# Kernel tuning notes

Measured on AMD Instinct MI355X. Metric: run time of the kernel, lower is better.

## Reference

```python
import jax, jax.numpy as jnp
import numpy as np

B, T, E, D, H = 32, 2048, 1024, 1024, 1024


def setup_inputs() -> dict:
    key = jax.random.key(0)
    ks = jax.random.split(key, 8)
    s_e = 1.0 / np.sqrt(E)
    s_d = 1.0 / np.sqrt(D)
    s_h = 1.0 / np.sqrt(H)
    return {
        "enc": jax.random.normal(ks[0], (B, T, E), dtype=jnp.float32),
        "dec": jax.random.normal(ks[1], (B, D), dtype=jnp.float32),
        "inp_mask": jnp.ones((B, T), dtype=jnp.float32),
        "W_enc": jax.random.uniform(ks[2], (E, H), jnp.float32, -s_e, s_e),
        "b_enc": jax.random.uniform(ks[3], (H,), jnp.float32, -s_e, s_e),
        "W_dec": jax.random.uniform(ks[4], (D, H), jnp.float32, -s_d, s_d),
        "b_dec": jax.random.uniform(ks[5], (H,), jnp.float32, -s_d, s_d),
        "w_out": jax.random.uniform(ks[6], (H,), jnp.float32, -s_h, s_h),
        "b_out": jax.random.uniform(ks[7], (), jnp.float32, -s_h, s_h),
    }


def reference(enc, dec, inp_mask, W_enc, b_enc, W_dec, b_dec, w_out, b_out):
    # hidden_enc: [B, T, H]; hidden_dec broadcast as query: [B, 1, H]
    hidden_enc = jnp.einsum("bte,eh->bth", enc, W_enc) + b_enc
    hidden_dec = dec @ W_dec + b_dec
    # additive attention score: tanh(h_enc + h_dec) . w_out + b_out -> [B, T]
    logits = jnp.tanh(hidden_enc + hidden_dec[:, None, :]) @ w_out + b_out
    logits = jnp.where(inp_mask > 0, logits, jnp.float32(-1e9))
    probs = jax.nn.softmax(logits, axis=-1)  # [B, T]
    attn = jnp.einsum("bt,bte->be", probs, enc)  # weighted sum of enc
    return attn, probs
```

## Files before the change

### kernel.cpp

```cpp
#include <hip/hip_runtime.h>

#define B_ 32
#define T_ 2048
#define E_ 1024
#define H_ 1024
#define M_ (B_*T_)

typedef __attribute__((ext_vector_type(8))) short short8;
typedef __attribute__((ext_vector_type(4))) float f32x4;


__device__ __forceinline__ void gload_lds16(const void* g, void* l) {
  __builtin_amdgcn_global_load_lds(
      (const __attribute__((address_space(1))) void*)g,
      (__attribute__((address_space(3))) void*)l, 16, 0, 0);
}

__device__ __forceinline__ short f2bf(float x) {
  unsigned u = __float_as_uint(x);
  unsigned r = (u + 0x7fffu + ((u >> 16) & 1u)) >> 16;
  return (short)r;
}

__device__ __forceinline__ float fast_tanh(float x) {
  float e = __expf(2.f * x);
  return 1.f - 2.f / (e + 1.f);
}


__global__ __launch_bounds__(256) void k0_wt(const float* __restrict__ W,
                                             unsigned short* __restrict__ Wt) {
  __shared__ float t[32][33];
  int e0 = (blockIdx.x >> 5) << 5;
  int h0 = (blockIdx.x & 31) << 5;
  int r = threadIdx.x >> 5, c = threadIdx.x & 31;
#pragma unroll
  for (int i = 0; i < 4; ++i)
    t[r + i*8][c] = W[(size_t)(e0 + r + i*8) * H_ + h0 + c];
  __syncthreads();
#pragma unroll
  for (int i = 0; i < 4; ++i)
    Wt[(size_t)(h0 + r + i*8) * E_ + e0 + c] = (unsigned short)f2bf(t[c][r + i*8]);
}


__global__ __launch_bounds__(256) void k1_cvec(const float* __restrict__ dec,
                                               const float* __restrict__ Wd,
                                               const float* __restrict__ b_enc,
                                               const float* __restrict__ b_dec,
                                               float* __restrict__ cvec) {
  __shared__ float ds[1024];
  int b = blockIdx.x >> 2, hb = blockIdx.x & 3;
  int tid = threadIdx.x;
#pragma unroll
  for (int i = 0; i < 4; ++i) ds[tid + i*256] = dec[b*1024 + tid + i*256];
  __syncthreads();
  int h = hb*256 + tid;
  float acc = b_enc[h] + b_dec[h];
#pragma unroll 8
  for (int d = 0; d < 1024; ++d) acc += ds[d] * Wd[(size_t)d * H_ + h];
  cvec[b*H_ + h] = acc;
}


__global__ __launch_bounds__(256) void k2_logits(
    const float* __restrict__ enc,
    const unsigned short* __restrict__ Wt,
    const float* __restrict__ cvec,
    const float* __restrict__ w_out,
    float* __restrict__ logits)
{
  __shared__ float ldsA[128*32];
  __shared__ unsigned short ldsB[128*32];

  const int tid  = threadIdx.x;
  const int wave = tid >> 6, lane = tid & 63;
  const int lr = lane & 15, lk = lane >> 4;
  const int wr = wave >> 1, wc = wave & 1;
  const int bm = blockIdx.x >> 3, bn = blockIdx.x & 7;

  const float* asrc[4];
  void* adst[4];
#pragma unroll
  for (int i = 0; i < 4; ++i) {
    int pos  = i*4096 + wave*1024 + lane*16;
    int row  = pos >> 7;
    int slot = (pos >> 4) & 7;
    int ks   = (slot ^ (row & 7)) * 4;
    asrc[i] = enc + (size_t)(bm*128 + row) * E_ + ks;
    adst[i] = (char*)ldsA + i*4096 + wave*1024;
  }
  const unsigned short* bsrc[2];
  void* bdst[2];
#pragma unroll
  for (int i = 0; i < 2; ++i) {
    int pos  = i*4096 + wave*1024 + lane*16;
    int nrow = pos >> 6;
    int ke   = (pos & 63) >> 1;
    bsrc[i] = Wt + (size_t)(bn*128 + nrow) * E_ + ke;
    bdst[i] = (char*)ldsB + i*4096 + wave*1024;
  }

  f32x4 acc[4][4];
  {
    f32x4 z = {0.f, 0.f, 0.f, 0.f};
#pragma unroll
    for (int mi = 0; mi < 4; ++mi)
#pragma unroll
      for (int ni = 0; ni < 4; ++ni) acc[mi][ni] = z;
  }

  for (int kt = 0; kt < E_/32; ++kt) {
    if (kt) __syncthreads();
#pragma unroll
    for (int i = 0; i < 4; ++i) gload_lds16(asrc[i] + kt*32, adst[i]);
#pragma unroll
    for (int i = 0; i < 2; ++i) gload_lds16(bsrc[i] + kt*32, bdst[i]);
    __syncthreads();

    short8 bfr[4];
#pragma unroll
    for (int ni = 0; ni < 4; ++ni) {
      int nrow = wc*64 + ni*16 + lr;
      bfr[ni] = *(const short8*)((const char*)ldsB + nrow*64 + lk*16);
    }
    short8 afr[4];
#pragma unroll
    for (int mi = 0; mi < 4; ++mi) {
      int row = wr*64 + mi*16 + lr;
      int s1 = (2*lk)     ^ (row & 7);
      int s2 = (2*lk + 1) ^ (row & 7);
      f32x4 f1 = *(const f32x4*)((const char*)ldsA + row*128 + s1*16);
      f32x4 f2 = *(const f32x4*)((const char*)ldsA + row*128 + s2*16);
      short8 a;
      a[0] = f2bf(f1[0]); a[1] = f2bf(f1[1]); a[2] = f2bf(f1[2]); a[3] = f2bf(f1[3]);
      a[4] = f2bf(f2[0]); a[5] = f2bf(f2[1]); a[6] = f2bf(f2[2]); a[7] = f2bf(f2[3]);
      afr[mi] = a;
    }
#pragma unroll
    for (int mi = 0; mi < 4; ++mi)
#pragma unroll
      for (int ni = 0; ni < 4; ++ni)
        acc[mi][ni] = __builtin_amdgcn_mfma_f32_16x16x32_bf16(
            afr[mi], bfr[ni], acc[mi][ni], 0, 0, 0);
  }

  const int bIdx = bm >> 4;
  float cv[4], wv[4];
#pragma unroll
  for (int ni = 0; ni < 4; ++ni) {
    int n = bn*128 + wc*64 + ni*16 + lr;
    cv[ni] = cvec[bIdx*H_ + n];
    wv[ni] = w_out[n];
  }
#pragma unroll
  for (int mi = 0; mi < 4; ++mi) {
#pragma unroll
    for (int r = 0; r < 4; ++r) {
      float s = 0.f;
#pragma unroll
      for (int ni = 0; ni < 4; ++ni) {
        float h = acc[mi][ni][r] + cv[ni];
        s += wv[ni] * fast_tanh(h);
      }
      s += __shfl_xor(s, 1);
      s += __shfl_xor(s, 2);
      s += __shfl_xor(s, 4);
      s += __shfl_xor(s, 8);
      if (lr == 0) {
        int m = bm*128 + wr*64 + mi*16 + lk*4 + r;
        atomicAdd(&logits[m], s);
      }
    }
  }
}


__global__ __launch_bounds__(256) void k3_softmax(
    const float* __restrict__ logits, const float* __restrict__ mask,
    const float* __restrict__ b_out, float* __restrict__ probs) {
  __shared__ float redm[4], reds[4];
  int b = blockIdx.x, tid = threadIdx.x;
  int wave = tid >> 6, lane = tid & 63;
  float bo = b_out[0];
  float lg[8];
  float mx = -1e30f;
#pragma unroll
  for (int i = 0; i < 8; ++i) {
    int t = i*256 + tid;
    float v = logits[b*T_ + t] + bo;
    v = (mask[b*T_ + t] > 0.f) ? v : -1e9f;
    lg[i] = v;
    mx = fmaxf(mx, v);
  }
#pragma unroll
  for (int off = 32; off; off >>= 1) mx = fmaxf(mx, __shfl_xor(mx, off));
  if (lane == 0) redm[wave] = mx;
  __syncthreads();
  mx = fmaxf(fmaxf(redm[0], redm[1]), fmaxf(redm[2], redm[3]));
  float sum = 0.f;
#pragma unroll
  for (int i = 0; i < 8; ++i) { lg[i] = __expf(lg[i] - mx); sum += lg[i]; }
#pragma unroll
  for (int off = 32; off; off >>= 1) sum += __shfl_xor(sum, off);
  if (lane == 0) reds[wave] = sum;
  __syncthreads();
  sum = reds[0] + reds[1] + reds[2] + reds[3];
  float inv = 1.f / sum;
#pragma unroll
  for (int i = 0; i < 8; ++i) {
    int t = i*256 + tid;
    probs[b*T_ + t] = lg[i] * inv;
  }
}


__global__ __launch_bounds__(256) void k4_attn(const float* __restrict__ enc,
                                               const float* __restrict__ probs,
                                               float* __restrict__ attn) {
  int bb = blockIdx.x >> 6;
  int t0 = (blockIdx.x & 63) * 32;
  int e0 = threadIdx.x * 4;
  float a0 = 0.f, a1 = 0.f, a2 = 0.f, a3 = 0.f;
#pragma unroll 4
  for (int tt = 0; tt < 32; ++tt) {
    int t = t0 + tt;
    float p = probs[bb*T_ + t];
    f32x4 v = *(const f32x4*)(enc + ((size_t)bb*T_ + t)*E_ + e0);
    a0 += p*v[0]; a1 += p*v[1]; a2 += p*v[2]; a3 += p*v[3];
  }
  atomicAdd(&attn[bb*E_ + e0 + 0], a0);
  atomicAdd(&attn[bb*E_ + e0 + 1], a1);
  atomicAdd(&attn[bb*E_ + e0 + 2], a2);
  atomicAdd(&attn[bb*E_ + e0 + 3], a3);
}


extern "C" void kernel_launch(void* const* d_in, const int* in_sizes, int n_in,
                              void* d_out, int out_size, void* d_ws, size_t ws_size,
                              hipStream_t stream) {
  const float* enc   = (const float*)d_in[0];
  const float* dec   = (const float*)d_in[1];
  const float* mask  = (const float*)d_in[2];
  const float* W_enc = (const float*)d_in[3];
  const float* b_enc = (const float*)d_in[4];
  const float* W_dec = (const float*)d_in[5];
  const float* b_dec = (const float*)d_in[6];
  const float* w_out = (const float*)d_in[7];
  const float* b_out = (const float*)d_in[8];

  float* out   = (float*)d_out;
  float* attn  = out;
  float* probs = out + B_*E_;

  char* ws = (char*)d_ws;
  unsigned short* Wt = (unsigned short*)ws;
  float* cvec   = (float*)(ws + (2u<<20));
  float* logits = (float*)(ws + (2u<<20) + (128u<<10));

  hipMemsetAsync(logits, 0, M_*sizeof(float), stream);
  hipMemsetAsync(attn,   0, B_*E_*sizeof(float), stream);

  k0_wt     <<<1024, 256, 0, stream>>>(W_enc, Wt);
  k1_cvec   <<< 128, 256, 0, stream>>>(dec, W_dec, b_enc, b_dec, cvec);
  k2_logits <<<4096, 256, 0, stream>>>(enc, Wt, cvec, w_out, logits);
  k3_softmax<<<  B_, 256, 0, stream>>>(logits, mask, b_out, probs);
  k4_attn   <<<2048, 256, 0, stream>>>(enc, probs, attn);
}
```

Measured before the change: 728.8 us.

## Pre-convert enc to bf16, widen K tile to 64, swizzle blocks, coarsen attn

Adds a pass that converts enc to bf16 in workspace when there is room. The logits GEMM then streams bf16 A tiles straight into LDS with a K step of 64, so per-tile fp32 loads and repeated in-loop conversion go away. Without room, a fallback converts in registers before storing to LDS. The change also remaps block order so consecutive blocks reuse the same Wt tile, and gives each attention block four times more rows so fewer atomics are needed. The extra conversion pass adds a full read of enc plus a bf16 write, which may cost more than it saves.

```diff
diff --git a/kernel.cpp b/kernel.cpp
--- a/kernel.cpp
+++ b/kernel.cpp
@@ -41,6 +41,21 @@
 #pragma unroll
   for (int i = 0; i < 4; ++i)
     Wt[(size_t)(h0 + r + i*8) * E_ + e0 + c] = (unsigned short)f2bf(t[c][r + i*8]);
+}
+
+
+__global__ __launch_bounds__(256) void k0b_cvt(const float* __restrict__ src,
+                                               unsigned short* __restrict__ dst) {
+  size_t base = ((size_t)blockIdx.x * 256 + threadIdx.x) * 16;
+  const f32x4* s = (const f32x4*)(src + base);
+  f32x4 a = s[0], b = s[1], c = s[2], d = s[3];
+  short8 r0, r1;
+  r0[0]=f2bf(a[0]); r0[1]=f2bf(a[1]); r0[2]=f2bf(a[2]); r0[3]=f2bf(a[3]);
+  r0[4]=f2bf(b[0]); r0[5]=f2bf(b[1]); r0[6]=f2bf(b[2]); r0[7]=f2bf(b[3]);
+  r1[0]=f2bf(c[0]); r1[1]=f2bf(c[1]); r1[2]=f2bf(c[2]); r1[3]=f2bf(c[3]);
+  r1[4]=f2bf(d[0]); r1[5]=f2bf(d[1]); r1[6]=f2bf(d[2]); r1[7]=f2bf(d[3]);
+  *(short8*)(dst + base)     = r0;
+  *(short8*)(dst + base + 8) = r1;
 }
 
 
@@ -63,41 +78,41 @@
 }
 
 
+template<bool PRECVT>
 __global__ __launch_bounds__(256) void k2_logits(
     const float* __restrict__ enc,
+    const unsigned short* __restrict__ encbf,
     const unsigned short* __restrict__ Wt,
     const float* __restrict__ cvec,
     const float* __restrict__ w_out,
     float* __restrict__ logits)
 {
-  __shared__ float ldsA[128*32];
-  __shared__ unsigned short ldsB[128*32];
+  __shared__ unsigned short ldsA[128*64];
+  __shared__ unsigned short ldsB[128*64];
 
   const int tid  = threadIdx.x;
   const int wave = tid >> 6, lane = tid & 63;
   const int lr = lane & 15, lk = lane >> 4;
   const int wr = wave >> 1, wc = wave & 1;
-  const int bm = blockIdx.x >> 3, bn = blockIdx.x & 7;
-
-  const float* asrc[4];
+
+  const int bid = blockIdx.x;
+  const int swz = (bid & 7) * 512 + (bid >> 3);
+  const int bm = swz >> 3, bn = swz & 7;
+
+  const unsigned short* asrc[4];
   void* adst[4];
+  const unsigned short* bsrc[4];
+  void* bdst[4];
 #pragma unroll
   for (int i = 0; i < 4; ++i) {
     int pos  = i*4096 + wave*1024 + lane*16;
     int row  = pos >> 7;
     int slot = (pos >> 4) & 7;
-    int ks   = (slot ^ (row & 7)) * 4;
-    asrc[i] = enc + (size_t)(bm*128 + row) * E_ + ks;
+    int klog = (slot ^ (row & 7)) * 8;
+    if (PRECVT)
+      asrc[i] = encbf + (size_t)(bm*128 + row) * E_ + klog;
+    bsrc[i] = Wt + (size_t)(bn*128 + row) * E_ + klog;
     adst[i] = (char*)ldsA + i*4096 + wave*1024;
-  }
-  const unsigned short* bsrc[2];
-  void* bdst[2];
-#pragma unroll
-  for (int i = 0; i < 2; ++i) {
-    int pos  = i*4096 + wave*1024 + lane*16;
-    int nrow = pos >> 6;
-    int ke   = (pos & 63) >> 1;
-    bsrc[i] = Wt + (size_t)(bn*128 + nrow) * E_ + ke;
     bdst[i] = (char*)ldsB + i*4096 + wave*1024;
   }
 
@@ -110,39 +125,51 @@
       for (int ni = 0; ni < 4; ++ni) acc[mi][ni] = z;
   }
 
-  for (int kt = 0; kt < E_/32; ++kt) {
+  for (int kt = 0; kt < E_/64; ++kt) {
     if (kt) __syncthreads();
 #pragma unroll
-    for (int i = 0; i < 4; ++i) gload_lds16(asrc[i] + kt*32, adst[i]);
-#pragma unroll
-    for (int i = 0; i < 2; ++i) gload_lds16(bsrc[i] + kt*32, bdst[i]);
+    for (int i = 0; i < 4; ++i) gload_lds16(bsrc[i] + kt*64, bdst[i]);
+    if constexpr (PRECVT) {
+#pragma unroll
+      for (int i = 0; i < 4; ++i) gload_lds16(asrc[i] + kt*64, adst[i]);
+    } else {
+#pragma unroll
+      for (int c = 0; c < 4; ++c) {
+        int chunk = tid + c*256;
+        int row = chunk >> 3, slot = chunk & 7;
+        const float* g = enc + (size_t)(bm*128 + row) * E_ + kt*64 + slot*8;
+        f32x4 f1 = *(const f32x4*)g;
+        f32x4 f2 = *(const f32x4*)(g + 4);
+        short8 a;
+        a[0]=f2bf(f1[0]); a[1]=f2bf(f1[1]); a[2]=f2bf(f1[2]); a[3]=f2bf(f1[3]);
+        a[4]=f2bf(f2[0]); a[5]=f2bf(f2[1]); a[6]=f2bf(f2[2]); a[7]=f2bf(f2[3]);
+        *(short8*)((char*)ldsA + row*128 + ((slot ^ (row & 7)) << 4)) = a;
+      }
+    }
     __syncthreads();
 
-    short8 bfr[4];
-#pragma unroll
-    for (int ni = 0; ni < 4; ++ni) {
-      int nrow = wc*64 + ni*16 + lr;
-      bfr[ni] = *(const short8*)((const char*)ldsB + nrow*64 + lk*16);
+#pragma unroll
+    for (int ks = 0; ks < 2; ++ks) {
+      short8 bfr[4], afr[4];
+#pragma unroll
+      for (int ni = 0; ni < 4; ++ni) {
+        int nrow = wc*64 + ni*16 + lr;
+        int ps = (ks*4 + lk) ^ (nrow & 7);
+        bfr[ni] = *(const short8*)((const char*)ldsB + nrow*128 + ps*16);
+      }
+#pragma unroll
+      for (int mi = 0; mi < 4; ++mi) {
+        int row = wr*64 + mi*16 + lr;
+        int ps = (ks*4 + lk) ^ (row & 7);
+        afr[mi] = *(const short8*)((const char*)ldsA + row*128 + ps*16);
+      }
+#pragma unroll
+      for (int mi = 0; mi < 4; ++mi)
+#pragma unroll
+        for (int ni = 0; ni < 4; ++ni)
+          acc[mi][ni] = __builtin_amdgcn_mfma_f32_16x16x32_bf16(
+              afr[mi], bfr[ni], acc[mi][ni], 0, 0, 0);
     }
-    short8 afr[4];
-#pragma unroll
-    for (int mi = 0; mi < 4; ++mi) {
-      int row = wr*64 + mi*16 + lr;
-      int s1 = (2*lk)     ^ (row & 7);
-      int s2 = (2*lk + 1) ^ (row & 7);
-      f32x4 f1 = *(const f32x4*)((const char*)ldsA + row*128 + s1*16);
-      f32x4 f2 = *(const f32x4*)((const char*)ldsA + row*128 + s2*16);
-      short8 a;
-      a[0] = f2bf(f1[0]); a[1] = f2bf(f1[1]); a[2] = f2bf(f1[2]); a[3] = f2bf(f1[3]);
-      a[4] = f2bf(f2[0]); a[5] = f2bf(f2[1]); a[6] = f2bf(f2[2]); a[7] = f2bf(f2[3]);
-      afr[mi] = a;
-    }
-#pragma unroll
-    for (int mi = 0; mi < 4; ++mi)
-#pragma unroll
-      for (int ni = 0; ni < 4; ++ni)
-        acc[mi][ni] = __builtin_amdgcn_mfma_f32_16x16x32_bf16(
-            afr[mi], bfr[ni], acc[mi][ni], 0, 0, 0);
   }
 
   const int bIdx = bm >> 4;
@@ -218,12 +245,12 @@
 __global__ __launch_bounds__(256) void k4_attn(const float* __restrict__ enc,
                                                const float* __restrict__ probs,
                                                float* __restrict__ attn) {
-  int bb = blockIdx.x >> 6;
-  int t0 = (blockIdx.x & 63) * 32;
+  int bb = blockIdx.x >> 4;
+  int t0 = (blockIdx.x & 15) * 128;
   int e0 = threadIdx.x * 4;
   float a0 = 0.f, a1 = 0.f, a2 = 0.f, a3 = 0.f;
 #pragma unroll 4
-  for (int tt = 0; tt < 32; ++tt) {
+  for (int tt = 0; tt < 128; ++tt) {
     int t = t0 + tt;
     float p = probs[bb*T_ + t];
     f32x4 v = *(const f32x4*)(enc + ((size_t)bb*T_ + t)*E_ + e0);
@@ -254,16 +281,25 @@
   float* probs = out + B_*E_;
 
   char* ws = (char*)d_ws;
-  unsigned short* Wt = (unsigned short*)ws;
-  float* cvec   = (float*)(ws + (2u<<20));
-  float* logits = (float*)(ws + (2u<<20) + (128u<<10));
+  size_t off = 0;
+  unsigned short* Wt = (unsigned short*)(ws + off);  off += (2u<<20);
+  float* cvec   = (float*)(ws + off);                off += (128u<<10);
+  float* logits = (float*)(ws + off);                off += (256u<<10);
+  unsigned short* encbf = (unsigned short*)(ws + off);
+  const size_t need = off + (size_t)M_ * E_ * 2;
+  const bool precvt = (ws_size >= need);
 
   hipMemsetAsync(logits, 0, M_*sizeof(float), stream);
   hipMemsetAsync(attn,   0, B_*E_*sizeof(float), stream);
 
-  k0_wt     <<<1024, 256, 0, stream>>>(W_enc, Wt);
-  k1_cvec   <<< 128, 256, 0, stream>>>(dec, W_dec, b_enc, b_dec, cvec);
-  k2_logits <<<4096, 256, 0, stream>>>(enc, Wt, cvec, w_out, logits);
+  k0_wt   <<<1024, 256, 0, stream>>>(W_enc, Wt);
+  k1_cvec <<< 128, 256, 0, stream>>>(dec, W_dec, b_enc, b_dec, cvec);
+  if (precvt) {
+    k0b_cvt <<<16384, 256, 0, stream>>>(enc, encbf);
+    k2_logits<true><<<4096, 256, 0, stream>>>(enc, encbf, Wt, cvec, w_out, logits);
+  } else {
+    k2_logits<false><<<4096, 256, 0, stream>>>(enc, encbf, Wt, cvec, w_out, logits);
+  }
   k3_softmax<<<  B_, 256, 0, stream>>>(logits, mask, b_out, probs);
-  k4_attn   <<<2048, 256, 0, stream>>>(enc, probs, attn);
-}
+  k4_attn   <<< 512, 256, 0, stream>>>(enc, probs, attn);
+}
```

After: 685.0 us. -6.0%, faster.
